# Kernel tuning notes

Measured on AMD Instinct MI355X. Metric: run time of the kernel, lower is better.

Reference implementation:

```python
import jax, jax.numpy as jnp
import numpy as np

N = 200000   # non-empty octree nodes
K = 27       # 3x3x3 neighborhood taps
C = 64       # channels (in == out, stride 1)
EPS = 1e-5


def octree_conv(x, neigh, W):
    # x: [N, Cin], neigh: [N, K] indices into rows of x, W: [K, Cin, Cout]
    g = x[neigh]                      # gather -> [N, K, Cin] (irregular access)
    return jnp.einsum('nkc,kcd->nd', g, W)


def batch_norm(x, gamma, beta):
    # training-mode BatchNorm1d over the node dimension
    mean = jnp.mean(x, axis=0)
    var = jnp.var(x, axis=0)
    return (x - mean) * jax.lax.rsqrt(var + EPS) * gamma + beta


def setup_inputs() -> dict:
    key = jax.random.key(0)
    ks = jax.random.split(key, 4)
    x = jax.random.normal(ks[0], (N, C), dtype=jnp.float32)
    neigh = jax.random.randint(ks[1], (N, K), 0, N, dtype=jnp.int64)
    scale = 1.0 / np.sqrt(K * C)
    W1 = jax.random.normal(ks[2], (K, C, C), dtype=jnp.float32) * scale
    W2 = jax.random.normal(ks[3], (K, C, C), dtype=jnp.float32) * scale
    return {
        'x': x, 'neigh': neigh, 'depth': 5,
        'W1': W1, 'gamma1': jnp.ones((C,), jnp.float32), 'beta1': jnp.zeros((C,), jnp.float32),
        'W2': W2, 'gamma2': jnp.ones((C,), jnp.float32), 'beta2': jnp.zeros((C,), jnp.float32),
    }


def reference(x, neigh, depth, W1, gamma1, beta1, W2, gamma2, beta2):
    residual = x
    out = octree_conv(x, neigh, W1)
    out = jax.nn.relu(batch_norm(out, gamma1, beta1))
    out = octree_conv(out, neigh, W2)   # stride == 1 -> same depth, same neighborhood
    out = batch_norm(out, gamma2, beta2)
    out = jax.nn.relu(out + residual)   # downsample is None for stride 1
    return (out, depth)
```

## Files before the change

### kernel.cpp

```cpp
#include <hip/hip_runtime.h>

typedef __attribute__((ext_vector_type(8))) short bf16x8;
typedef __attribute__((ext_vector_type(4))) float f32x4;

static __device__ __forceinline__ unsigned short f2bf(float f) {
    unsigned int u = __builtin_bit_cast(unsigned int, f);
    u += 0x7fffu + ((u >> 16) & 1u);
    return (unsigned short)(u >> 16);
}
static __device__ __forceinline__ float bf2f(unsigned short h) {
    unsigned int u = ((unsigned int)h) << 16;
    return __builtin_bit_cast(float, u);
}

__global__ void cvt_xw_kernel(const float* __restrict__ x, unsigned short* __restrict__ xb, int total8, int gx,
                              const float* __restrict__ w1, const float* __restrict__ w2,
                              unsigned short* __restrict__ wt1, unsigned short* __restrict__ wt2) {
    if ((int)blockIdx.x < gx) {
        int i = blockIdx.x * 256 + threadIdx.x;
        if (i >= total8) return;
        const float4* p = reinterpret_cast<const float4*>(x) + (size_t)i * 2;
        float4 a = p[0], b = p[1];
        bf16x8 o;
        o[0] = (short)f2bf(a.x); o[1] = (short)f2bf(a.y); o[2] = (short)f2bf(a.z); o[3] = (short)f2bf(a.w);
        o[4] = (short)f2bf(b.x); o[5] = (short)f2bf(b.y); o[6] = (short)f2bf(b.z); o[7] = (short)f2bf(b.w);
        reinterpret_cast<bf16x8*>(xb)[i] = o;
    } else {
        int i = (blockIdx.x - gx) * 256 + threadIdx.x;
        if (i >= 2 * 27 * 4096) return;
        const float* w = (i < 27 * 4096) ? w1 : w2;
        unsigned short* wt = (i < 27 * 4096) ? wt1 : wt2;
        int j = (i < 27 * 4096) ? i : i - 27 * 4096;
        int k = j >> 12;
        int cout = (j >> 6) & 63;
        int cin = j & 63;
        wt[j] = f2bf(w[((size_t)(k * 64 + cin)) * 64 + cout]);
    }
}

__global__ __launch_bounds__(256, 5) void conv_mfma(
    const unsigned short* __restrict__ xb,
    const int* __restrict__ nh,
    const unsigned short* __restrict__ wt,
    unsigned short* __restrict__ y,
    float* __restrict__ pS,
    float* __restrict__ pQ,
    int n)
{
    __shared__ unsigned short Atile[3][4096];
    __shared__ int lidx[27 * 64];

    const int tid  = threadIdx.x;
    const int wid  = tid >> 6;
    const int lane = tid & 63;
    const int lr   = lane & 15;
    const int lg   = lane >> 4;
    const int base = blockIdx.x * 64;

    for (int j = tid; j < 27 * 64; j += 256) {
        int row = j / 27;
        int kk  = j - row * 27;
        int gr  = base + row; if (gr >= n) gr = n - 1;
        lidx[j] = nh[(size_t)gr * 27 + kk];
    }
    __syncthreads();

    const int srow = tid >> 3;
    const int xoff = ((tid & 7) ^ (srow & 7)) * 8;
    const int so0  = srow * 27;
    const int so1  = (srow + 32) * 27;

    f32x4 acc[4];
    #pragma unroll
    for (int t = 0; t < 4; ++t) acc[t] = (f32x4){0.f, 0.f, 0.f, 0.f};

    const unsigned short* wB = wt + (wid * 16 + lr) * 64 + lg * 8;
    bf16x8 Ba0, Ba1, Bb0, Bb1, Bc0, Bc1;

#define ISSUE(kk, BUF, B0, B1) do {                                                   \
        const int i0_ = lidx[so0 + (kk)];                                             \
        const int i1_ = lidx[so1 + (kk)];                                             \
        B0 = *reinterpret_cast<const bf16x8*>(wB + (size_t)(kk) * 4096);              \
        B1 = *reinterpret_cast<const bf16x8*>(wB + (size_t)(kk) * 4096 + 32);         \
        __builtin_amdgcn_global_load_lds(                                             \
            (const __attribute__((address_space(1))) unsigned int*)(xb + (size_t)i0_ * 64 + xoff), \
            (__attribute__((address_space(3))) unsigned int*)(&Atile[BUF][wid * 512]), 16, 0, 0);    \
        __builtin_amdgcn_global_load_lds(                                             \
            (const __attribute__((address_space(1))) unsigned int*)(xb + (size_t)i1_ * 64 + xoff), \
            (__attribute__((address_space(3))) unsigned int*)(&Atile[BUF][2048 + wid * 512]), 16, 0, 0); \
    } while (0)

#define PHASE(BUF, B0, B1, VMSTR) do {                                                \
        asm volatile("s_waitcnt " VMSTR ::: "memory");                                \
        __builtin_amdgcn_s_barrier();                                                 \
        __builtin_amdgcn_sched_barrier(0);                                            \
        const unsigned short* At = &Atile[BUF][0];                                    \
        _Pragma("unroll")                                                             \
        for (int t = 0; t < 4; ++t) {                                                 \
            const int row_ = t * 16 + lr;                                             \
            const int sw_  = (row_ & 7) * 8;                                          \
            bf16x8 A0 = *reinterpret_cast<const bf16x8*>(&At[row_ * 64 + ((lg * 8) ^ sw_)]);        \
            bf16x8 A1 = *reinterpret_cast<const bf16x8*>(&At[row_ * 64 + (((4 + lg) * 8) ^ sw_)]);  \
            acc[t] = __builtin_amdgcn_mfma_f32_16x16x32_bf16(A0, B0, acc[t], 0, 0, 0); \
            acc[t] = __builtin_amdgcn_mfma_f32_16x16x32_bf16(A1, B1, acc[t], 0, 0, 0); \
        }                                                                             \
        asm volatile("s_waitcnt lgkmcnt(0)" ::: "memory");                            \
        __builtin_amdgcn_sched_barrier(0);                                            \
        __builtin_amdgcn_s_barrier();                                                 \
    } while (0)

    ISSUE(0, 0, Ba0, Ba1);
    ISSUE(1, 1, Bb0, Bb1);

    #pragma unroll 1
    for (int k = 0; k < 24; k += 3) {
        ISSUE(k + 2, 2, Bc0, Bc1);
        PHASE(0, Ba0, Ba1, "vmcnt(8)");
        ISSUE(k + 3, 0, Ba0, Ba1);
        PHASE(1, Bb0, Bb1, "vmcnt(8)");
        ISSUE(k + 4, 1, Bb0, Bb1);
        PHASE(2, Bc0, Bc1, "vmcnt(8)");
    }
    ISSUE(26, 2, Bc0, Bc1);
    PHASE(0, Ba0, Ba1, "vmcnt(8)");
    PHASE(1, Bb0, Bb1, "vmcnt(4)");
    PHASE(2, Bc0, Bc1, "vmcnt(0)");
#undef ISSUE
#undef PHASE

    float s1 = 0.f, s2 = 0.f;
    #pragma unroll
    for (int t = 0; t < 4; ++t) {
        #pragma unroll
        for (int rg = 0; rg < 4; ++rg) {
            const int row = base + t * 16 + lg * 4 + rg;
            if (row < n) {
                const float v = acc[t][rg];
                s1 += v;
                s2 += v * v;
            }
        }
    }
    s1 += __shfl_xor(s1, 16); s1 += __shfl_xor(s1, 32);
    s2 += __shfl_xor(s2, 16); s2 += __shfl_xor(s2, 32);
    if (lane < 16) {
        const int ch = wid * 16 + lane;
        pS[(size_t)ch * gridDim.x + blockIdx.x] = s1;
        pQ[(size_t)ch * gridDim.x + blockIdx.x] = s2;
    }

    unsigned short* yt = &Atile[0][0];
    #pragma unroll
    for (int t = 0; t < 4; ++t) {
        #pragma unroll
        for (int rg = 0; rg < 4; ++rg) {
            const int row = t * 16 + lg * 4 + rg;
            const int ch  = (wid * 2 + (lr >> 3)) ^ (row & 7);
            yt[row * 64 + ch * 8 + (lr & 7)] = f2bf(acc[t][rg]);
        }
    }
    __syncthreads();
    {
        const int r0 = tid >> 3;
        const int j  = tid & 7;
        const int g0 = base + r0;
        const int g1 = base + 32 + r0;
        bf16x8 v0 = *reinterpret_cast<const bf16x8*>(&yt[r0 * 64 + ((j ^ (r0 & 7)) * 8)]);
        if (g0 < n) *reinterpret_cast<bf16x8*>(&y[(size_t)g0 * 64 + j * 8]) = v0;
        bf16x8 v1 = *reinterpret_cast<const bf16x8*>(&yt[(32 + r0) * 64 + ((j ^ (r0 & 7)) * 8)]);
        if (g1 < n) *reinterpret_cast<bf16x8*>(&y[(size_t)g1 * 64 + j * 8]) = v1;
    }
}

__global__ __launch_bounds__(256) void bn_stats_kernel(
        const float* __restrict__ pS, const float* __restrict__ pQ,
        const float* __restrict__ gamma, const float* __restrict__ beta,
        float* __restrict__ bnp, int nb, float invN) {
    const int c = blockIdx.x;
    const int tid = threadIdx.x;
    float S = 0.f, Q = 0.f;
    for (int b = tid; b < nb; b += 256) {
        S += pS[(size_t)c * nb + b];
        Q += pQ[(size_t)c * nb + b];
    }
    #pragma unroll
    for (int o = 1; o < 64; o <<= 1) {
        S += __shfl_xor(S, o);
        Q += __shfl_xor(Q, o);
    }
    __shared__ float sh[8];
    if ((tid & 63) == 0) { sh[(tid >> 6) * 2] = S; sh[(tid >> 6) * 2 + 1] = Q; }
    __syncthreads();
    if (tid == 0) {
        S = sh[0] + sh[2] + sh[4] + sh[6];
        Q = sh[1] + sh[3] + sh[5] + sh[7];
        const float mean = S * invN;
        const float var  = Q * invN - mean * mean;
        const float sc   = gamma[c] * rsqrtf(var + 1e-5f);
        bnp[c]      = sc;
        bnp[64 + c] = beta[c] - mean * sc;
    }
}

__global__ void bn_relu_kernel(const unsigned short* __restrict__ y, const float* __restrict__ bnp,
                               unsigned short* __restrict__ yn, int total8) {
    int i = blockIdx.x * blockDim.x + threadIdx.x;
    if (i >= total8) return;
    bf16x8 v = reinterpret_cast<const bf16x8*>(y)[i];
    int c0 = (i * 8) & 63;
    bf16x8 o;
    #pragma unroll
    for (int j = 0; j < 8; ++j) {
        float f = bf2f((unsigned short)v[j]) * bnp[c0 + j] + bnp[64 + c0 + j];
        f = fmaxf(f, 0.f);
        o[j] = (short)f2bf(f);
    }
    reinterpret_cast<bf16x8*>(yn)[i] = o;
}

__global__ void final_kernel(const unsigned short* __restrict__ y2, const float* __restrict__ x,
                             const float* __restrict__ bnp, const int* __restrict__ depth,
                             float* __restrict__ out, int total8, int n) {
    int i = blockIdx.x * blockDim.x + threadIdx.x;
    if (i == 0) out[(size_t)n * 64] = (float)depth[0];
    if (i >= total8) return;
    bf16x8 v = reinterpret_cast<const bf16x8*>(y2)[i];
    const float4* xp = reinterpret_cast<const float4*>(x) + (size_t)i * 2;
    float4 xa = xp[0], xbv = xp[1];
    int c0 = (i * 8) & 63;
    float r[8];
    #pragma unroll
    for (int j = 0; j < 8; ++j)
        r[j] = bf2f((unsigned short)v[j]) * bnp[c0 + j] + bnp[64 + c0 + j];
    r[0] += xa.x;  r[1] += xa.y;  r[2] += xa.z;  r[3] += xa.w;
    r[4] += xbv.x; r[5] += xbv.y; r[6] += xbv.z; r[7] += xbv.w;
    float4* op = reinterpret_cast<float4*>(out) + (size_t)i * 2;
    float4 o0 = {fmaxf(r[0], 0.f), fmaxf(r[1], 0.f), fmaxf(r[2], 0.f), fmaxf(r[3], 0.f)};
    float4 o1 = {fmaxf(r[4], 0.f), fmaxf(r[5], 0.f), fmaxf(r[6], 0.f), fmaxf(r[7], 0.f)};
    op[0] = o0;
    op[1] = o1;
}

extern "C" void kernel_launch(void* const* d_in, const int* in_sizes, int n_in,
                              void* d_out, int out_size, void* d_ws, size_t ws_size,
                              hipStream_t stream) {
    const float* x     = (const float*)d_in[0];
    const int*   neigh = (const int*)d_in[1];
    const int*   depth = (const int*)d_in[2];
    const float* W1    = (const float*)d_in[3];
    const float* g1    = (const float*)d_in[4];
    const float* b1    = (const float*)d_in[5];
    const float* W2    = (const float*)d_in[6];
    const float* g2    = (const float*)d_in[7];
    const float* b2    = (const float*)d_in[8];
    float* out = (float*)d_out;

    const int n      = in_sizes[0] / 64;
    const int total8 = in_sizes[0] / 8;
    const int nb     = (n + 63) / 64;

    char* ws = (char*)d_ws;
    size_t off = 0;
    auto carve = [&](size_t bytes) -> char* {
        char* p = ws + off;
        off += (bytes + 255) & ~((size_t)255);
        return p;
    };
    unsigned short* bufA = (unsigned short*)carve((size_t)n * 64 * 2);
    unsigned short* bufB = (unsigned short*)carve((size_t)n * 64 * 2);
    unsigned short* w1t  = (unsigned short*)carve(27 * 4096 * 2);
    unsigned short* w2t  = (unsigned short*)carve(27 * 4096 * 2);
    float*          pS   = (float*)carve((size_t)nb * 64 * 4);
    float*          pQ   = (float*)carve((size_t)nb * 64 * 4);
    float*          bnp1 = (float*)carve(128 * 4);
    float*          bnp2 = (float*)carve(128 * 4);

    const int gx   = (total8 + 255) / 256;
    const int gw   = (2 * 27 * 4096 + 255) / 256;
    const float invN = 1.0f / (float)n;

    cvt_xw_kernel<<<gx + gw, 256, 0, stream>>>(x, bufA, total8, gx, W1, W2, w1t, w2t);

    conv_mfma<<<nb, 256, 0, stream>>>(bufA, neigh, w1t, bufB, pS, pQ, n);
    bn_stats_kernel<<<64, 256, 0, stream>>>(pS, pQ, g1, b1, bnp1, nb, invN);
    bn_relu_kernel<<<gx, 256, 0, stream>>>(bufB, bnp1, bufA, total8);

    conv_mfma<<<nb, 256, 0, stream>>>(bufA, neigh, w2t, bufB, pS, pQ, n);
    bn_stats_kernel<<<64, 256, 0, stream>>>(pS, pQ, g2, b2, bnp2, nb, invN);
    final_kernel<<<gx, 256, 0, stream>>>(bufB, x, bnp2, depth, out, total8, n);
}
```

Baseline: 278.2 us.

## Quantize gathered activations to int8 with per-row scales to halve gather traffic

Activations are stored as int8 with a per-node scale, so each neighbor gather moves 64 bytes instead of 128. The conv kernel now stages weights in LDS via async loads and loads A rows straight into registers. It expands the int8 values to bf16 in registers, runs the MFMA per tap and applies the per-row scale when accumulating. BN statistics are reduced across waves in LDS, and BN+ReLU is fused with requantization. This costs accuracy from 8-bit activations, extra conversion ALU work per tap and more scalar scale loads.

```diff
diff --git a/kernel.cpp b/kernel.cpp
--- a/kernel.cpp
+++ b/kernel.cpp
@@ -2,6 +2,8 @@
 
 typedef __attribute__((ext_vector_type(8))) short bf16x8;
 typedef __attribute__((ext_vector_type(4))) float f32x4;
+typedef __attribute__((ext_vector_type(4))) int   i32x4;
+typedef __attribute__((ext_vector_type(4))) unsigned int u32x4;
 
 static __device__ __forceinline__ unsigned short f2bf(float f) {
     unsigned int u = __builtin_bit_cast(unsigned int, f);
@@ -13,42 +15,54 @@
     return __builtin_bit_cast(float, u);
 }
 
-__global__ void cvt_xw_kernel(const float* __restrict__ x, unsigned short* __restrict__ xb, int total8, int gx,
-                              const float* __restrict__ w1, const float* __restrict__ w2,
-                              unsigned short* __restrict__ wt1, unsigned short* __restrict__ wt2) {
-    if ((int)blockIdx.x < gx) {
-        int i = blockIdx.x * 256 + threadIdx.x;
-        if (i >= total8) return;
-        const float4* p = reinterpret_cast<const float4*>(x) + (size_t)i * 2;
-        float4 a = p[0], b = p[1];
-        bf16x8 o;
-        o[0] = (short)f2bf(a.x); o[1] = (short)f2bf(a.y); o[2] = (short)f2bf(a.z); o[3] = (short)f2bf(a.w);
-        o[4] = (short)f2bf(b.x); o[5] = (short)f2bf(b.y); o[6] = (short)f2bf(b.z); o[7] = (short)f2bf(b.w);
-        reinterpret_cast<bf16x8*>(xb)[i] = o;
-    } else {
-        int i = (blockIdx.x - gx) * 256 + threadIdx.x;
-        if (i >= 2 * 27 * 4096) return;
-        const float* w = (i < 27 * 4096) ? w1 : w2;
-        unsigned short* wt = (i < 27 * 4096) ? wt1 : wt2;
-        int j = (i < 27 * 4096) ? i : i - 27 * 4096;
-        int k = j >> 12;
-        int cout = (j >> 6) & 63;
-        int cin = j & 63;
-        wt[j] = f2bf(w[((size_t)(k * 64 + cin)) * 64 + cout]);
-    }
-}
-
-__global__ __launch_bounds__(256, 5) void conv_mfma(
-    const unsigned short* __restrict__ xb,
+__global__ void qx_kernel(const float* __restrict__ x, signed char* __restrict__ xq,
+                          float* __restrict__ sc, int n) {
+    const int m = blockIdx.x * 32 + (threadIdx.x >> 3);
+    const int j = threadIdx.x & 7;
+    if (m >= n) return;
+    const float4* p = reinterpret_cast<const float4*>(x + (size_t)m * 64 + j * 8);
+    float4 a = p[0], b = p[1];
+    float mx = fmaxf(fmaxf(fmaxf(fabsf(a.x), fabsf(a.y)), fmaxf(fabsf(a.z), fabsf(a.w))),
+                     fmaxf(fmaxf(fabsf(b.x), fabsf(b.y)), fmaxf(fabsf(b.z), fabsf(b.w))));
+    mx = fmaxf(mx, __shfl_xor(mx, 1));
+    mx = fmaxf(mx, __shfl_xor(mx, 2));
+    mx = fmaxf(mx, __shfl_xor(mx, 4));
+    const float inv = mx > 0.f ? 127.0f / mx : 0.f;
+    auto qb = [&](float f, int sh) -> unsigned long long {
+        int t = (int)rintf(f * inv);
+        t = t < -127 ? -127 : (t > 127 ? 127 : t);
+        return ((unsigned long long)(unsigned char)(signed char)t) << sh;
+    };
+    unsigned long long pk = qb(a.x, 0) | qb(a.y, 8) | qb(a.z, 16) | qb(a.w, 24)
+                          | qb(b.x, 32) | qb(b.y, 40) | qb(b.z, 48) | qb(b.w, 56);
+    const int dst = (j < 4) ? j * 16 : (j - 4) * 16 + 8;
+    *reinterpret_cast<unsigned long long*>(xq + (size_t)m * 64 + dst) = pk;
+    if (j == 0) sc[m] = mx * (1.0f / 127.0f);
+}
+
+__global__ void cvt_w_kernel(const float* __restrict__ w1, const float* __restrict__ w2,
+                             unsigned short* __restrict__ wt1, unsigned short* __restrict__ wt2) {
+    int i = blockIdx.x * blockDim.x + threadIdx.x;
+    if (i >= 2 * 27 * 4096) return;
+    const float* w = (i < 27 * 4096) ? w1 : w2;
+    unsigned short* wt = (i < 27 * 4096) ? wt1 : wt2;
+    int j = (i < 27 * 4096) ? i : i - 27 * 4096;
+    int k = j >> 12;
+    int cout = (j >> 6) & 63;
+    int cin = j & 63;
+    wt[j] = f2bf(w[((size_t)(k * 64 + cin)) * 64 + cout]);
+}
+
+__global__ __launch_bounds__(256, 4) void conv_i8a(
+    const signed char* __restrict__ xq,
+    const float* __restrict__ scx,
     const int* __restrict__ nh,
     const unsigned short* __restrict__ wt,
     unsigned short* __restrict__ y,
-    float* __restrict__ pS,
-    float* __restrict__ pQ,
-    int n)
+    float* __restrict__ pS, float* __restrict__ pQ, int n)
 {
-    __shared__ unsigned short Atile[3][4096];
-    __shared__ int lidx[27 * 64];
+    __shared__ unsigned short Bbuf[3][4096];
+    __shared__ int lidx[64 * 27];
 
     const int tid  = threadIdx.x;
     const int wid  = tid >> 6;
@@ -57,7 +71,7 @@
     const int lg   = lane >> 4;
     const int base = blockIdx.x * 64;
 
-    for (int j = tid; j < 27 * 64; j += 256) {
+    for (int j = tid; j < 64 * 27; j += 256) {
         int row = j / 27;
         int kk  = j - row * 27;
         int gr  = base + row; if (gr >= n) gr = n - 1;
@@ -65,98 +79,130 @@
     }
     __syncthreads();
 
-    const int srow = tid >> 3;
-    const int xoff = ((tid & 7) ^ (srow & 7)) * 8;
-    const int so0  = srow * 27;
-    const int so1  = (srow + 32) * 27;
+    const int aoff = (wid * 16 + lr) * 27;
+    const int d0o  = (wid * 16 + lg * 4 + 0) * 27;
+    const int d1o  = (wid * 16 + lg * 4 + 1) * 27;
+    const int d2o  = (wid * 16 + lg * 4 + 2) * 27;
+    const int d3o  = (wid * 16 + lg * 4 + 3) * 27;
+    const int bs   = (wid * 16 + (lane >> 3)) * 64 + (((lane & 7) ^ ((lane >> 3) & 7)) << 3);
 
     f32x4 acc[4];
     #pragma unroll
     for (int t = 0; t < 4; ++t) acc[t] = (f32x4){0.f, 0.f, 0.f, 0.f};
-
-    const unsigned short* wB = wt + (wid * 16 + lr) * 64 + lg * 8;
-    bf16x8 Ba0, Ba1, Bb0, Bb1, Bc0, Bc1;
-
-#define ISSUE(kk, BUF, B0, B1) do {                                                   \
-        const int i0_ = lidx[so0 + (kk)];                                             \
-        const int i1_ = lidx[so1 + (kk)];                                             \
-        B0 = *reinterpret_cast<const bf16x8*>(wB + (size_t)(kk) * 4096);              \
-        B1 = *reinterpret_cast<const bf16x8*>(wB + (size_t)(kk) * 4096 + 32);         \
+    const f32x4 fz = (f32x4){0.f, 0.f, 0.f, 0.f};
+
+    i32x4 RAa, RAb, RAc;
+    float Da0,Da1,Da2,Da3, Db0,Db1,Db2,Db3, Dc0,Dc1,Dc2,Dc3;
+
+#define ISSUE(kk, BUF, RA, D0, D1, D2, D3) do {                                       \
         __builtin_amdgcn_global_load_lds(                                             \
-            (const __attribute__((address_space(1))) unsigned int*)(xb + (size_t)i0_ * 64 + xoff), \
-            (__attribute__((address_space(3))) unsigned int*)(&Atile[BUF][wid * 512]), 16, 0, 0);    \
+            (const __attribute__((address_space(1))) unsigned int*)(wt + (size_t)(kk)*4096 + bs), \
+            (__attribute__((address_space(3))) unsigned int*)(&Bbuf[BUF][wid * 1024]), 16, 0, 0); \
         __builtin_amdgcn_global_load_lds(                                             \
-            (const __attribute__((address_space(1))) unsigned int*)(xb + (size_t)i1_ * 64 + xoff), \
-            (__attribute__((address_space(3))) unsigned int*)(&Atile[BUF][2048 + wid * 512]), 16, 0, 0); \
+            (const __attribute__((address_space(1))) unsigned int*)(wt + (size_t)(kk)*4096 + bs + 512), \
+            (__attribute__((address_space(3))) unsigned int*)(&Bbuf[BUF][wid * 1024 + 512]), 16, 0, 0); \
+        RA = *reinterpret_cast<const i32x4*>(xq + (size_t)lidx[aoff + (kk)] * 64 + (lg << 4)); \
+        D0 = scx[lidx[d0o + (kk)]];                                                   \
+        D1 = scx[lidx[d1o + (kk)]];                                                   \
+        D2 = scx[lidx[d2o + (kk)]];                                                   \
+        D3 = scx[lidx[d3o + (kk)]];                                                   \
     } while (0)
 
-#define PHASE(BUF, B0, B1, VMSTR) do {                                                \
+#define EXP4(W, O0, O1) do {                                                          \
+        int w_ = (W);                                                                 \
+        float f0_ = (float)((w_ << 24) >> 24);                                        \
+        float f1_ = (float)((w_ << 16) >> 24);                                        \
+        float f2_ = (float)((w_ << 8) >> 24);                                         \
+        float f3_ = (float)(w_ >> 24);                                                \
+        O0 = (__builtin_bit_cast(unsigned int, f0_) >> 16) | (__builtin_bit_cast(unsigned int, f1_) & 0xffff0000u); \
+        O1 = (__builtin_bit_cast(unsigned int, f2_) >> 16) | (__builtin_bit_cast(unsigned int, f3_) & 0xffff0000u); \
+    } while (0)
+
+#define PHASE(BUF, RA, D0, D1, D2, D3, VMSTR) do {                                    \
         asm volatile("s_waitcnt " VMSTR ::: "memory");                                \
         __builtin_amdgcn_s_barrier();                                                 \
         __builtin_amdgcn_sched_barrier(0);                                            \
-        const unsigned short* At = &Atile[BUF][0];                                    \
+        unsigned int e0,e1,e2,e3,e4,e5,e6,e7;                                         \
+        EXP4(RA[0], e0, e1); EXP4(RA[1], e2, e3);                                     \
+        EXP4(RA[2], e4, e5); EXP4(RA[3], e6, e7);                                     \
+        u32x4 ah0_ = (u32x4){e0,e1,e2,e3};                                            \
+        u32x4 ah1_ = (u32x4){e4,e5,e6,e7};                                            \
+        bf16x8 Ah0 = __builtin_bit_cast(bf16x8, ah0_);                                \
+        bf16x8 Ah1 = __builtin_bit_cast(bf16x8, ah1_);                                \
+        const unsigned short* Bt = &Bbuf[BUF][0];                                     \
         _Pragma("unroll")                                                             \
-        for (int t = 0; t < 4; ++t) {                                                 \
-            const int row_ = t * 16 + lr;                                             \
-            const int sw_  = (row_ & 7) * 8;                                          \
-            bf16x8 A0 = *reinterpret_cast<const bf16x8*>(&At[row_ * 64 + ((lg * 8) ^ sw_)]);        \
-            bf16x8 A1 = *reinterpret_cast<const bf16x8*>(&At[row_ * 64 + (((4 + lg) * 8) ^ sw_)]);  \
-            acc[t] = __builtin_amdgcn_mfma_f32_16x16x32_bf16(A0, B0, acc[t], 0, 0, 0); \
-            acc[t] = __builtin_amdgcn_mfma_f32_16x16x32_bf16(A1, B1, acc[t], 0, 0, 0); \
+        for (int ct = 0; ct < 4; ++ct) {                                              \
+            const int br_ = (ct * 16 + lr) * 64;                                      \
+            bf16x8 B0 = *reinterpret_cast<const bf16x8*>(&Bt[br_ + ((lg ^ (lr & 7)) << 3)]);        \
+            bf16x8 B1 = *reinterpret_cast<const bf16x8*>(&Bt[br_ + (((4 + lg) ^ (lr & 7)) << 3)]);  \
+            f32x4 Sf = __builtin_amdgcn_mfma_f32_16x16x32_bf16(Ah0, B0, fz, 0, 0, 0); \
+            Sf = __builtin_amdgcn_mfma_f32_16x16x32_bf16(Ah1, B1, Sf, 0, 0, 0);       \
+            acc[ct][0] += Sf[0] * D0;                                                 \
+            acc[ct][1] += Sf[1] * D1;                                                 \
+            acc[ct][2] += Sf[2] * D2;                                                 \
+            acc[ct][3] += Sf[3] * D3;                                                 \
         }                                                                             \
         asm volatile("s_waitcnt lgkmcnt(0)" ::: "memory");                            \
         __builtin_amdgcn_sched_barrier(0);                                            \
         __builtin_amdgcn_s_barrier();                                                 \
     } while (0)
 
-    ISSUE(0, 0, Ba0, Ba1);
-    ISSUE(1, 1, Bb0, Bb1);
+    ISSUE(0, 0, RAa, Da0, Da1, Da2, Da3);
+    __builtin_amdgcn_sched_barrier(0);
+    ISSUE(1, 1, RAb, Db0, Db1, Db2, Db3);
+    __builtin_amdgcn_sched_barrier(0);
 
     #pragma unroll 1
     for (int k = 0; k < 24; k += 3) {
-        ISSUE(k + 2, 2, Bc0, Bc1);
-        PHASE(0, Ba0, Ba1, "vmcnt(8)");
-        ISSUE(k + 3, 0, Ba0, Ba1);
-        PHASE(1, Bb0, Bb1, "vmcnt(8)");
-        ISSUE(k + 4, 1, Bb0, Bb1);
-        PHASE(2, Bc0, Bc1, "vmcnt(8)");
-    }
-    ISSUE(26, 2, Bc0, Bc1);
-    PHASE(0, Ba0, Ba1, "vmcnt(8)");
-    PHASE(1, Bb0, Bb1, "vmcnt(4)");
-    PHASE(2, Bc0, Bc1, "vmcnt(0)");
+        ISSUE(k + 2, 2, RAc, Dc0, Dc1, Dc2, Dc3);
+        PHASE(0, RAa, Da0, Da1, Da2, Da3, "vmcnt(14)");
+        ISSUE(k + 3, 0, RAa, Da0, Da1, Da2, Da3);
+        PHASE(1, RAb, Db0, Db1, Db2, Db3, "vmcnt(14)");
+        ISSUE(k + 4, 1, RAb, Db0, Db1, Db2, Db3);
+        PHASE(2, RAc, Dc0, Dc1, Dc2, Dc3, "vmcnt(14)");
+    }
+    ISSUE(26, 2, RAc, Dc0, Dc1, Dc2, Dc3);
+    PHASE(0, RAa, Da0, Da1, Da2, Da3, "vmcnt(14)");
+    PHASE(1, RAb, Db0, Db1, Db2, Db3, "vmcnt(7)");
+    PHASE(2, RAc, Dc0, Dc1, Dc2, Dc3, "vmcnt(0)");
 #undef ISSUE
 #undef PHASE
-
-    float s1 = 0.f, s2 = 0.f;
-    #pragma unroll
-    for (int t = 0; t < 4; ++t) {
+#undef EXP4
+
+    float s1[4] = {0.f,0.f,0.f,0.f}, s2[4] = {0.f,0.f,0.f,0.f};
+    #pragma unroll
+    for (int ct = 0; ct < 4; ++ct) {
         #pragma unroll
         for (int rg = 0; rg < 4; ++rg) {
-            const int row = base + t * 16 + lg * 4 + rg;
+            const int row = base + wid * 16 + lg * 4 + rg;
             if (row < n) {
-                const float v = acc[t][rg];
-                s1 += v;
-                s2 += v * v;
+                const float v = acc[ct][rg];
+                s1[ct] += v;
+                s2[ct] += v * v;
             }
         }
     }
-    s1 += __shfl_xor(s1, 16); s1 += __shfl_xor(s1, 32);
-    s2 += __shfl_xor(s2, 16); s2 += __shfl_xor(s2, 32);
+    #pragma unroll
+    for (int ct = 0; ct < 4; ++ct) {
+        s1[ct] += __shfl_xor(s1[ct], 16); s1[ct] += __shfl_xor(s1[ct], 32);
+        s2[ct] += __shfl_xor(s2[ct], 16); s2[ct] += __shfl_xor(s2[ct], 32);
+    }
+    unsigned short* yt = &Bbuf[0][0];
+    float* fs = reinterpret_cast<float*>(&Bbuf[2][0]);
     if (lane < 16) {
-        const int ch = wid * 16 + lane;
-        pS[(size_t)ch * gridDim.x + blockIdx.x] = s1;
-        pQ[(size_t)ch * gridDim.x + blockIdx.x] = s2;
-    }
-
-    unsigned short* yt = &Atile[0][0];
-    #pragma unroll
-    for (int t = 0; t < 4; ++t) {
+        #pragma unroll
+        for (int ct = 0; ct < 4; ++ct) {
+            fs[(ct * 16 + lr) * 4 + wid]       = s1[ct];
+            fs[256 + (ct * 16 + lr) * 4 + wid] = s2[ct];
+        }
+    }
+    #pragma unroll
+    for (int ct = 0; ct < 4; ++ct) {
         #pragma unroll
         for (int rg = 0; rg < 4; ++rg) {
-            const int row = t * 16 + lg * 4 + rg;
-            const int ch  = (wid * 2 + (lr >> 3)) ^ (row & 7);
-            yt[row * 64 + ch * 8 + (lr & 7)] = f2bf(acc[t][rg]);
+            const int row = wid * 16 + lg * 4 + rg;
+            const int ch  = (ct * 2 + (lr >> 3)) ^ (row & 7);
+            yt[row * 64 + ch * 8 + (lr & 7)] = f2bf(acc[ct][rg]);
         }
     }
     __syncthreads();
@@ -169,6 +215,12 @@
         if (g0 < n) *reinterpret_cast<bf16x8*>(&y[(size_t)g0 * 64 + j * 8]) = v0;
         bf16x8 v1 = *reinterpret_cast<const bf16x8*>(&yt[(32 + r0) * 64 + ((j ^ (r0 & 7)) * 8)]);
         if (g1 < n) *reinterpret_cast<bf16x8*>(&y[(size_t)g1 * 64 + j * 8]) = v1;
+    }
+    if (tid < 64) {
+        const float S = fs[tid * 4] + fs[tid * 4 + 1] + fs[tid * 4 + 2] + fs[tid * 4 + 3];
+        const float Q = fs[256 + tid * 4] + fs[256 + tid * 4 + 1] + fs[256 + tid * 4 + 2] + fs[256 + tid * 4 + 3];
+        pS[(size_t)tid * gridDim.x + blockIdx.x] = S;
+        pQ[(size_t)tid * gridDim.x + blockIdx.x] = Q;
     }
 }
 
@@ -202,20 +254,35 @@
     }
 }
 
-__global__ void bn_relu_kernel(const unsigned short* __restrict__ y, const float* __restrict__ bnp,
-                               unsigned short* __restrict__ yn, int total8) {
-    int i = blockIdx.x * blockDim.x + threadIdx.x;
-    if (i >= total8) return;
-    bf16x8 v = reinterpret_cast<const bf16x8*>(y)[i];
-    int c0 = (i * 8) & 63;
-    bf16x8 o;
-    #pragma unroll
-    for (int j = 0; j < 8; ++j) {
-        float f = bf2f((unsigned short)v[j]) * bnp[c0 + j] + bnp[64 + c0 + j];
-        f = fmaxf(f, 0.f);
-        o[j] = (short)f2bf(f);
-    }
-    reinterpret_cast<bf16x8*>(yn)[i] = o;
+__global__ void qbn_kernel(const unsigned short* __restrict__ y, const float* __restrict__ bnp,
+                           signed char* __restrict__ yq, float* __restrict__ sc, int n) {
+    const int m = blockIdx.x * 32 + (threadIdx.x >> 3);
+    const int j = threadIdx.x & 7;
+    if (m >= n) return;
+    bf16x8 v = *reinterpret_cast<const bf16x8*>(y + (size_t)m * 64 + j * 8);
+    float f[8];
+    #pragma unroll
+    for (int e = 0; e < 8; ++e) {
+        const int c = j * 8 + e;
+        float t = bf2f((unsigned short)v[e]) * bnp[c] + bnp[64 + c];
+        f[e] = fmaxf(t, 0.f);
+    }
+    float mx = fmaxf(fmaxf(fmaxf(f[0], f[1]), fmaxf(f[2], f[3])),
+                     fmaxf(fmaxf(f[4], f[5]), fmaxf(f[6], f[7])));
+    mx = fmaxf(mx, __shfl_xor(mx, 1));
+    mx = fmaxf(mx, __shfl_xor(mx, 2));
+    mx = fmaxf(mx, __shfl_xor(mx, 4));
+    const float inv = mx > 0.f ? 127.0f / mx : 0.f;
+    unsigned long long pk = 0;
+    #pragma unroll
+    for (int e = 0; e < 8; ++e) {
+        int t = (int)rintf(f[e] * inv);
+        t = t < -127 ? -127 : (t > 127 ? 127 : t);
+        pk |= ((unsigned long long)(unsigned char)(signed char)t) << (8 * e);
+    }
+    const int dst = (j < 4) ? j * 16 : (j - 4) * 16 + 8;
+    *reinterpret_cast<unsigned long long*>(yq + (size_t)m * 64 + dst) = pk;
+    if (j == 0) sc[m] = mx * (1.0f / 127.0f);
 }
 
 __global__ void final_kernel(const unsigned short* __restrict__ y2, const float* __restrict__ x,
@@ -266,8 +333,9 @@
         off += (bytes + 255) & ~((size_t)255);
         return p;
     };
-    unsigned short* bufA = (unsigned short*)carve((size_t)n * 64 * 2);
-    unsigned short* bufB = (unsigned short*)carve((size_t)n * 64 * 2);
+    signed char*    xq   = (signed char*)carve((size_t)n * 64);
+    float*          scx  = (float*)carve((size_t)n * 4);
+    unsigned short* y1   = (unsigned short*)carve((size_t)n * 64 * 2);
     unsigned short* w1t  = (unsigned short*)carve(27 * 4096 * 2);
     unsigned short* w2t  = (unsigned short*)carve(27 * 4096 * 2);
     float*          pS   = (float*)carve((size_t)nb * 64 * 4);
@@ -275,17 +343,19 @@
     float*          bnp1 = (float*)carve(128 * 4);
     float*          bnp2 = (float*)carve(128 * 4);
 
-    const int gx   = (total8 + 255) / 256;
-    const int gw   = (2 * 27 * 4096 + 255) / 256;
+    const int gq  = (n + 31) / 32;
+    const int gw  = (2 * 27 * 4096 + 255) / 256;
+    const int gx  = (total8 + 255) / 256;
     const float invN = 1.0f / (float)n;
 
-    cvt_xw_kernel<<<gx + gw, 256, 0, stream>>>(x, bufA, total8, gx, W1, W2, w1t, w2t);
-
-    conv_mfma<<<nb, 256, 0, stream>>>(bufA, neigh, w1t, bufB, pS, pQ, n);
+    qx_kernel<<<gq, 256, 0, stream>>>(x, xq, scx, n);
+    cvt_w_kernel<<<gw, 256, 0, stream>>>(W1, W2, w1t, w2t);
+
+    conv_i8a<<<nb, 256, 0, stream>>>(xq, scx, neigh, w1t, y1, pS, pQ, n);
     bn_stats_kernel<<<64, 256, 0, stream>>>(pS, pQ, g1, b1, bnp1, nb, invN);
-    bn_relu_kernel<<<gx, 256, 0, stream>>>(bufB, bnp1, bufA, total8);
-
-    conv_mfma<<<nb, 256, 0, stream>>>(bufA, neigh, w2t, bufB, pS, pQ, n);
+    qbn_kernel<<<gq, 256, 0, stream>>>(y1, bnp1, xq, scx, n);
+
+    conv_i8a<<<nb, 256, 0, stream>>>(xq, scx, neigh, w2t, y1, pS, pQ, n);
     bn_stats_kernel<<<64, 256, 0, stream>>>(pS, pQ, g2, b2, bnp2, nb, invN);
-    final_kernel<<<gx, 256, 0, stream>>>(bufB, x, bnp2, depth, out, total8, n);
-}
+    final_kernel<<<gx, 256, 0, stream>>>(y1, x, bnp2, depth, out, total8, n);
+}
```

Result: slower. 292.8 us (+5.3%).
